# Kernel optimization log

Measured on AMD Instinct MI355X. Metric: run time of the kernel, lower is better.

Reference implementation:

```python
import jax, jax.numpy as jnp
import numpy as np

N_DIRS = 32  # number of projection directions


def gram_schmidt(x):
    # x: [B, n, D]; sequential Gram-Schmidt; normalized basis vectors are
    # detached (stop_gradient) as in the torch original.
    B, n, D = x.shape
    xs = jnp.swapaxes(x, 0, 1)  # [n, B, D]
    basis0 = jnp.zeros((n, B, D), dtype=x.dtype)

    def step(carry, w):
        basis, i = carry

        def proj(j, wv):
            b = basis[j]  # rows >= i are zero and contribute nothing
            return wv - b * jnp.sum(wv * b, axis=-1, keepdims=True)

        w_o = jax.lax.fori_loop(0, n, proj, w)
        w_sg = jax.lax.stop_gradient(w_o)
        w_hat = w_sg / jnp.linalg.norm(w_sg, axis=-1, keepdims=True)
        basis = jax.lax.dynamic_update_slice(basis, w_hat[None], (i, 0, 0))
        return (basis, i + 1), w_o

    (_, _), x_orth = jax.lax.scan(step, (basis0, jnp.int32(0)), xs)
    return jnp.swapaxes(x_orth, 0, 1)  # [B, n, D]


def setup_inputs() -> dict:
    key = jax.random.key(0)
    k = jax.random.split(key, 6)
    B = 2048
    IN_LP = 32 * 26       # 832 = linear_projection_x_dim * 26
    IMG = 28 * 28         # 784
    IN_NET = 2 * IMG      # 1568
    OUT_NET = N_DIRS * IMG  # 25088

    x_distorted = jax.random.normal(k[0], (B, IN_LP), dtype=jnp.float32)
    x_restored = jax.random.uniform(k[1], (B, 1, 28, 28), dtype=jnp.float32)

    s1 = 1.0 / np.sqrt(IN_LP)
    W_lp = jax.random.uniform(k[2], (IMG, IN_LP), jnp.float32, -s1, s1)
    b_lp = jax.random.uniform(k[3], (IMG,), jnp.float32, -s1, s1)

    s2 = 1.0 / np.sqrt(IN_NET)
    W_net = jax.random.uniform(k[4], (OUT_NET, IN_NET), jnp.float32, -s2, s2)
    b_net = jax.random.uniform(k[5], (OUT_NET,), jnp.float32, -s2, s2)

    return {"x_distorted": x_distorted, "x_restored": x_restored,
            "W_lp": W_lp, "b_lp": b_lp, "W_net": W_net, "b_net": b_net}


def reference(x_distorted, x_restored, W_lp, b_lp, W_net, b_net):
    B = x_distorted.shape[0]
    xd = x_distorted.reshape(B, -1) @ W_lp.T + b_lp      # [B, 784]
    xd = xd.reshape(B, 1, 28, 28)
    x = jnp.concatenate([xd, x_restored], axis=1)        # [B, 2, 28, 28]
    x = (x - 0.5) / 0.2
    w_mat = (x.reshape(B, -1) @ W_net.T + b_net) * 0.2   # [B, n_dirs*784]
    w_mat = w_mat.reshape(B, N_DIRS, -1)                 # [B, n_dirs, 784]
    return gram_schmidt(w_mat)
```

## Files before the change

kernel.cpp:

```cpp
#include <hip/hip_runtime.h>
#include <hip/hip_bf16.h>
#include <stdint.h>


typedef short s16x8 __attribute__((ext_vector_type(8)));
typedef float f32x4 __attribute__((ext_vector_type(4)));

#define GL_LDS16(gptr, lptr)                                                   \
    __builtin_amdgcn_global_load_lds(                                          \
        (const __attribute__((address_space(1))) void*)(gptr),                 \
        (__attribute__((address_space(3))) void*)(lptr), 16, 0, 0)

#define KP 1600

__global__ __launch_bounds__(512, 1) void gemm_mfma_256(
    const __hip_bfloat16* __restrict__ A, const __hip_bfloat16* __restrict__ B,
    const float* __restrict__ bias, float* __restrict__ C,
    int M, int N, int K)
{
    __shared__ __align__(16) short lds[2][32768];

    const int t = threadIdx.x;
    const int l = t & 63;
    const int wv = t >> 6;
    const int wm = wv >> 2;
    const int wn = wv & 3;

    const int f  = blockIdx.x;
    const int xb = f >> 3;
    const int yb = f & 7;
    const int m0 = yb * 256;
    const int n0 = xb * 256;

    const short* As = (const short*)A;
    const short* Bs = (const short*)B;

    const int colE = (((l & 7) ^ (l >> 3)) << 3);
    const size_t aSrc0 = (size_t)(m0 +   0 + wv * 8 + (l >> 3)) * KP + colE;
    const size_t aSrc1 = (size_t)(m0 + 128 + wv * 8 + (l >> 3)) * KP + colE;
    const size_t bSrc0 = (size_t)(n0 +   0 + wv * 8 + (l >> 3)) * KP + colE;
    const size_t bSrc1 = (size_t)(n0 + 128 + wv * 8 + (l >> 3)) * KP + colE;
    const int dstW = wv * 512;

    const int sk0 = (((l >> 4) << 3)) ^ ((l & 7) << 3);
    const int sk1 = sk0 ^ 32;
    const int aBase = wm * 8192 + (l & 15) * 64;
    const int bBase = 16384 + (wn >> 1) * 8192 +
                      ((wn & 1) * 64 + (l & 15)) * 64;

    f32x4 acc[8][4] = {};

#define STAGE_TILE(buf, T)                                                     \
    do {                                                                       \
        short* d_ = &lds[buf][0];                                              \
        const size_t ko_ = (size_t)(T) * 64;                                   \
        GL_LDS16(As + aSrc0 + ko_,            d_ + dstW);                      \
        GL_LDS16(As + aSrc0 + 64 * KP + ko_,  d_ + dstW + 4096);               \
        GL_LDS16(As + aSrc1 + ko_,            d_ + dstW + 8192);               \
        GL_LDS16(As + aSrc1 + 64 * KP + ko_,  d_ + dstW + 12288);              \
        GL_LDS16(Bs + bSrc0 + ko_,            d_ + dstW + 16384);              \
        GL_LDS16(Bs + bSrc0 + 64 * KP + ko_,  d_ + dstW + 20480);              \
        GL_LDS16(Bs + bSrc1 + ko_,            d_ + dstW + 24576);              \
        GL_LDS16(Bs + bSrc1 + 64 * KP + ko_,  d_ + dstW + 28672);              \
    } while (0)

    const int NT = K >> 6;
    STAGE_TILE(0, 0);
    __syncthreads();

    for (int kt = 0; kt < NT; ++kt) {
        const int cur = kt & 1;
        const short* bufc = &lds[cur][0];

        if (kt + 1 < NT) STAGE_TILE(cur ^ 1, kt + 1);

        s16x8 bfr[4][2];
        #pragma unroll
        for (int ni = 0; ni < 4; ++ni) {
            bfr[ni][0] = *(const s16x8*)&bufc[bBase + ni * 1024 + sk0];
            bfr[ni][1] = *(const s16x8*)&bufc[bBase + ni * 1024 + sk1];
        }

        #pragma unroll
        for (int half = 0; half < 2; ++half) {
            s16x8 afr[4][2];
            #pragma unroll
            for (int mi = 0; mi < 4; ++mi) {
                const int ro = (half * 64 + mi * 16) * 64;
                afr[mi][0] = *(const s16x8*)&bufc[aBase + ro + sk0];
                afr[mi][1] = *(const s16x8*)&bufc[aBase + ro + sk1];
            }
            __builtin_amdgcn_s_setprio(1);
            #pragma unroll
            for (int mi = 0; mi < 4; ++mi)
                #pragma unroll
                for (int ni = 0; ni < 4; ++ni) {
                    acc[half * 4 + mi][ni] =
                        __builtin_amdgcn_mfma_f32_16x16x32_bf16(
                            afr[mi][0], bfr[ni][0], acc[half * 4 + mi][ni],
                            0, 0, 0);
                    acc[half * 4 + mi][ni] =
                        __builtin_amdgcn_mfma_f32_16x16x32_bf16(
                            afr[mi][1], bfr[ni][1], acc[half * 4 + mi][ni],
                            0, 0, 0);
                }
            __builtin_amdgcn_s_setprio(0);
        }

        __syncthreads();
    }
#undef STAGE_TILE

    const int row0 = m0 + wm * 128 + ((l >> 4) << 2);
    const int col0 = n0 + wn * 64 + (l & 15);
    #pragma unroll
    for (int ni = 0; ni < 4; ++ni) {
        const int n = col0 + ni * 16;
        const float bn = bias[n];
        #pragma unroll
        for (int mi = 0; mi < 8; ++mi) {
            const int r0 = row0 + mi * 16;
            #pragma unroll
            for (int r = 0; r < 4; ++r)
                C[(size_t)(r0 + r) * N + n] = (acc[mi][ni][r] + bn) * 0.2f;
        }
    }
}

__global__ __launch_bounds__(256) void wnet_to_bf16(
    const float* __restrict__ in, __hip_bfloat16* __restrict__ out)
{
    const size_t r = blockIdx.x;
    const int t = threadIdx.x;
    const float* src = in + r * 1568;
    __hip_bfloat16* dst = out + r * KP;

    for (int i = t; i < 392; i += 256) {
        float4 v = *(const float4*)(src + (i << 2));
        __hip_bfloat16 o[4] = {
            __float2bfloat16(v.x), __float2bfloat16(v.y),
            __float2bfloat16(v.z), __float2bfloat16(v.w)};
        *(ushort4*)&dst[i << 2] = *(const ushort4*)o;
    }
    if (t < 8)
        *(ushort4*)&dst[1568 + (t << 2)] = make_ushort4(0, 0, 0, 0);
}

#define TILE_M 64
#define TILE_N 64
#define TILE_K 16
#define LDS_STRIDE 72

__global__ __launch_bounds__(256) void gemm_nt_lp(
    const float* __restrict__ A, const float* __restrict__ B,
    const float* __restrict__ bias, __hip_bfloat16* __restrict__ C,
    int M, int N, int K, int ldc)
{
    __shared__ float As[TILE_K][LDS_STRIDE];
    __shared__ float Bsh[TILE_K][LDS_STRIDE];

    const int t  = threadIdx.x;
    const int tx = t & 15;
    const int ty = t >> 4;
    const int m0 = blockIdx.y * TILE_M;
    const int n0 = blockIdx.x * TILE_N;
    const int lrow = t >> 2;
    const int lk   = (t & 3) << 2;

    float acc[4][4] = {};

    for (int kt = 0; kt < K; kt += TILE_K) {
        float4 av = *(const float4*)(A + (size_t)(m0 + lrow) * K + kt + lk);
        float4 bv = make_float4(0.f, 0.f, 0.f, 0.f);
        if (n0 + lrow < N)
            bv = *(const float4*)(B + (size_t)(n0 + lrow) * K + kt + lk);

        __syncthreads();
        As[lk + 0][lrow] = av.x; As[lk + 1][lrow] = av.y;
        As[lk + 2][lrow] = av.z; As[lk + 3][lrow] = av.w;
        Bsh[lk + 0][lrow] = bv.x; Bsh[lk + 1][lrow] = bv.y;
        Bsh[lk + 2][lrow] = bv.z; Bsh[lk + 3][lrow] = bv.w;
        __syncthreads();

        #pragma unroll
        for (int k = 0; k < TILE_K; ++k) {
            float4 a = *(const float4*)&As[k][ty << 2];
            float4 b = *(const float4*)&Bsh[k][tx << 2];
            acc[0][0] += a.x * b.x; acc[0][1] += a.x * b.y;
            acc[0][2] += a.x * b.z; acc[0][3] += a.x * b.w;
            acc[1][0] += a.y * b.x; acc[1][1] += a.y * b.y;
            acc[1][2] += a.y * b.z; acc[1][3] += a.y * b.w;
            acc[2][0] += a.z * b.x; acc[2][1] += a.z * b.y;
            acc[2][2] += a.z * b.z; acc[2][3] += a.z * b.w;
            acc[3][0] += a.w * b.x; acc[3][1] += a.w * b.y;
            acc[3][2] += a.w * b.z; acc[3][3] += a.w * b.w;
        }
    }

    #pragma unroll
    for (int j = 0; j < 4; ++j) {
        int n = n0 + (tx << 2) + j;
        if (n < N) {
            float bn = bias[n];
            #pragma unroll
            for (int i = 0; i < 4; ++i) {
                float v = (acc[i][j] + bn - 0.5f) / 0.2f;
                C[(size_t)(m0 + (ty << 2) + i) * ldc + n] = __float2bfloat16(v);
            }
        }
    }
}

__global__ __launch_bounds__(256) void build_restored(
    const float* __restrict__ xr, __hip_bfloat16* __restrict__ x)
{
    const int b = blockIdx.x;
    const int t = threadIdx.x;
    if (t < 196) {
        float4 v = *(const float4*)(xr + (size_t)b * 784 + (t << 2));
        __hip_bfloat16 o[4] = {
            __float2bfloat16((v.x - 0.5f) / 0.2f),
            __float2bfloat16((v.y - 0.5f) / 0.2f),
            __float2bfloat16((v.z - 0.5f) / 0.2f),
            __float2bfloat16((v.w - 0.5f) / 0.2f)};
        *(ushort4*)&x[(size_t)b * KP + 784 + (t << 2)] = *(const ushort4*)o;
    } else if (t < 204) {
        *(ushort4*)&x[(size_t)b * KP + 1568 + ((t - 196) << 2)] =
            make_ushort4(0, 0, 0, 0);
    }
}

#define GS_N 32
#define GS_D 784

__global__ __launch_bounds__(256, 4) void gram_solve(
    const float* __restrict__ out, float* __restrict__ Mws)
{
    __shared__ __align__(16) short Wc[GS_N * 64];
    __shared__ float Gs[GS_N][GS_N + 1];
    __shared__ float Ms[GS_N][GS_N + 1];
    __shared__ float Ld[GS_N];

    const int t = threadIdx.x;
    const int l = t & 63;
    const int w = t >> 6;
    const float* row0 = out + (size_t)blockIdx.x * (GS_N * GS_D);

    const int wr = w >> 1, wc2 = w & 1;
    const int ra = wr * 16 + (l & 15);
    const int rb = wc2 * 16 + (l & 15);
    const int kg = l >> 4;

    f32x4 acc = {};

    for (int k0 = 0; k0 < 832; k0 += 64) {
        #pragma unroll
        for (int hh = 0; hh < 2; ++hh) {
            const int h   = t + hh * 256;
            const int r   = h >> 4;
            const int hg  = h & 15;
            const int col = k0 + (hg << 2);
            ushort4 u = make_ushort4(0, 0, 0, 0);
            if (col < GS_D) {
                float4 v = *(const float4*)(row0 + r * GS_D + col);
                __hip_bfloat16 hb[4] = {
                    __float2bfloat16(v.x), __float2bfloat16(v.y),
                    __float2bfloat16(v.z), __float2bfloat16(v.w)};
                u = *(const ushort4*)hb;
            }
            const int gp = (hg >> 1) ^ (r & 7);
            *(ushort4*)&Wc[(r << 6) + (gp << 3) + ((hg & 1) << 2)] = u;
        }
        __syncthreads();

        #pragma unroll
        for (int s = 0; s < 2; ++s) {
            const int ga = ((s << 2) + kg) ^ (ra & 7);
            const int gb = ((s << 2) + kg) ^ (rb & 7);
            s16x8 af = *(const s16x8*)&Wc[(ra << 6) + (ga << 3)];
            s16x8 bf = *(const s16x8*)&Wc[(rb << 6) + (gb << 3)];
            acc = __builtin_amdgcn_mfma_f32_16x16x32_bf16(af, bf, acc, 0, 0, 0);
        }
        __syncthreads();
    }

    {
        const int di = wr * 16 + (l >> 4) * 4;
        const int dj = wc2 * 16 + (l & 15);
        #pragma unroll
        for (int r = 0; r < 4; ++r) Gs[di + r][dj] = acc[r];
    }
    for (int z = t; z < GS_N * (GS_N + 1); z += 256) ((float*)Ms)[z] = 0.f;
    __syncthreads();

    for (int k = 0; k < GS_N; ++k) {
        const float sk = sqrtf(Gs[k][k]);
        if (t == k) Ld[k] = sk;
        if (t > k && t < GS_N) Gs[t][k] /= sk;
        __syncthreads();
        if (t > k && t < GS_N) {
            const float lik = Gs[t][k];
            for (int j = k + 1; j <= t; ++j)
                Gs[t][j] -= lik * Gs[j][k];
        }
        __syncthreads();
    }

    if (t < GS_N) {
        const int j = t;
        Ms[j][j] = 1.0f / Ld[j];
        for (int i = j + 1; i < GS_N; ++i) {
            float a = 0.f;
            for (int k = j; k < i; ++k)
                a += Gs[i][k] * Ms[k][j];
            Ms[i][j] = -a / Ld[i];
        }
        for (int i = j + 1; i < GS_N; ++i)
            Ms[i][j] *= Ld[i];
    }
    __syncthreads();

    {
        const int i = t >> 3, j0 = (t & 7) << 2;
        float4 mv = make_float4(Ms[i][j0], Ms[i][j0 + 1],
                                Ms[i][j0 + 2], Ms[i][j0 + 3]);
        *(float4*)(Mws + (size_t)blockIdx.x * 1024 + (t << 2)) = mv;
    }
}

__global__ __launch_bounds__(256, 8) void gs_apply(
    float* __restrict__ out, const float* __restrict__ Mws)
{
    __shared__ float4 Wf[GS_N][28];
    __shared__ float  Ml[GS_N][36];

    const int t = threadIdx.x;
    const int b = blockIdx.y;
    const int k0 = blockIdx.x * 112;
    float* row0 = out + (size_t)b * (GS_N * GS_D);

    {
        float4 mv = *(const float4*)(Mws + (size_t)b * 1024 + (t << 2));
        const int i = t >> 3, j0 = (t & 7) << 2;
        *(float4*)&Ml[i][j0] = mv;
    }
    #pragma unroll
    for (int hh = 0; hh < 4; ++hh) {
        const int h = t + hh * 256;
        const int r = h >> 5, c = h & 31;
        if (c < 28)
            Wf[r][c] = *(const float4*)(row0 + r * GS_D + k0 + (c << 2));
    }
    __syncthreads();

    const int rg = t >> 5;
    const int c4 = t & 31;
    if (c4 < 28) {
        const int i0 = rg << 2;
        float4 c0 = Wf[i0 + 0][c4];
        float4 c1 = Wf[i0 + 1][c4];
        float4 c2 = Wf[i0 + 2][c4];
        float4 c3 = Wf[i0 + 3][c4];
        for (int j = 0; j < GS_N - 1; ++j) {
            if (j > i0 + 2) break;
            const float4 wj = Wf[j][c4];
            const float m0 = (i0 + 0 > j) ? Ml[i0 + 0][j] : 0.f;
            const float m1 = (i0 + 1 > j) ? Ml[i0 + 1][j] : 0.f;
            const float m2 = (i0 + 2 > j) ? Ml[i0 + 2][j] : 0.f;
            const float m3 = (i0 + 3 > j) ? Ml[i0 + 3][j] : 0.f;
            c0.x += m0 * wj.x; c0.y += m0 * wj.y;
            c0.z += m0 * wj.z; c0.w += m0 * wj.w;
            c1.x += m1 * wj.x; c1.y += m1 * wj.y;
            c1.z += m1 * wj.z; c1.w += m1 * wj.w;
            c2.x += m2 * wj.x; c2.y += m2 * wj.y;
            c2.z += m2 * wj.z; c2.w += m2 * wj.w;
            c3.x += m3 * wj.x; c3.y += m3 * wj.y;
            c3.z += m3 * wj.z; c3.w += m3 * wj.w;
        }
        *(float4*)(row0 + (i0 + 0) * GS_D + k0 + (c4 << 2)) = c0;
        *(float4*)(row0 + (i0 + 1) * GS_D + k0 + (c4 << 2)) = c1;
        *(float4*)(row0 + (i0 + 2) * GS_D + k0 + (c4 << 2)) = c2;
        *(float4*)(row0 + (i0 + 3) * GS_D + k0 + (c4 << 2)) = c3;
    }
}

extern "C" void kernel_launch(void* const* d_in, const int* in_sizes, int n_in,
                              void* d_out, int out_size, void* d_ws, size_t ws_size,
                              hipStream_t stream)
{
    const float* xd   = (const float*)d_in[0];
    const float* xr   = (const float*)d_in[1];
    const float* Wlp  = (const float*)d_in[2];
    const float* blp  = (const float*)d_in[3];
    const float* Wnet = (const float*)d_in[4];
    const float* bnet = (const float*)d_in[5];
    float* out = (float*)d_out;

    const int B = 2048, IN_LP = 832, IMG = 784, OUT = 32 * 784;

    __hip_bfloat16* Wnet_bf = (__hip_bfloat16*)d_ws;
    __hip_bfloat16* x_bf =
        (__hip_bfloat16*)((char*)d_ws + (size_t)OUT * KP * 2);
    float* Mws = (float*)d_ws;

    wnet_to_bf16<<<OUT, 256, 0, stream>>>(Wnet, Wnet_bf);

    gemm_nt_lp<<<dim3((IMG + TILE_N - 1) / TILE_N, B / TILE_M), 256, 0, stream>>>(
        xd, Wlp, blp, x_bf, B, IMG, IN_LP, KP);

    build_restored<<<B, 256, 0, stream>>>(xr, x_bf);

    gemm_mfma_256<<<dim3(784), 512, 0, stream>>>(
        x_bf, Wnet_bf, bnet, out, B, OUT, KP);

    gram_solve<<<B, 256, 0, stream>>>(out, Mws);

    gs_apply<<<dim3(7, B), 256, 0, stream>>>(out, Mws);
}
```

Baseline: 455.7 us.

## Retile main GEMM to 256x224 blocks and balance triangular GS apply work

Changes the big MFMA GEMM tile from 256x256 to 256x224, so N=25088 splits into 112 column blocks and the grid becomes 896 blocks. Warps are rearranged as 4x2 with 64x112 sub-tiles, and the A and B loads are split so half the waves stage A and half stage B. The gs_apply kernel now pairs rows i with 31-i so each thread gets a balanced share of the triangular update, instead of giving the bottom row groups more work. This trades some per-block reuse and adds a tail of extra blocks for finer tiling, aiming for better CU balance (896 blocks on 256 CUs) and less divergence.

After: 448.1 us. About the same (-1.7%).

```diff
diff --git a/kernel.cpp b/kernel.cpp
--- a/kernel.cpp
+++ b/kernel.cpp
@@ -18,50 +18,50 @@
     const float* __restrict__ bias, float* __restrict__ C,
     int M, int N, int K)
 {
-    __shared__ __align__(16) short lds[2][32768];
+    __shared__ __align__(16) short lds[2][30720];
 
     const int t = threadIdx.x;
     const int l = t & 63;
     const int wv = t >> 6;
-    const int wm = wv >> 2;
-    const int wn = wv & 3;
+    const int wm = wv >> 1;
+    const int wn = wv & 1;
 
     const int f  = blockIdx.x;
     const int xb = f >> 3;
     const int yb = f & 7;
     const int m0 = yb * 256;
-    const int n0 = xb * 256;
+    const int n0 = xb * 224;
 
     const short* As = (const short*)A;
     const short* Bs = (const short*)B;
 
+    const bool isA = wv < 4;
     const int colE = (((l & 7) ^ (l >> 3)) << 3);
-    const size_t aSrc0 = (size_t)(m0 +   0 + wv * 8 + (l >> 3)) * KP + colE;
-    const size_t aSrc1 = (size_t)(m0 + 128 + wv * 8 + (l >> 3)) * KP + colE;
-    const size_t bSrc0 = (size_t)(n0 +   0 + wv * 8 + (l >> 3)) * KP + colE;
-    const size_t bSrc1 = (size_t)(n0 + 128 + wv * 8 + (l >> 3)) * KP + colE;
-    const int dstW = wv * 512;
-
-    const int sk0 = (((l >> 4) << 3)) ^ ((l & 7) << 3);
+    const size_t srcRow = isA ? (size_t)(m0 + wv * 64 + (l >> 3))
+                              : (size_t)(n0 + (wv - 4) * 56 + (l >> 3));
+    const size_t src0 = srcRow * KP + colE;
+    const short* gsrc = isA ? As : Bs;
+    const int dstBase = isA ? wv * 4096 : 16384 + (wv - 4) * 3584;
+
+    const int sk0 = ((l >> 4) << 3) ^ ((l & 7) << 3);
     const int sk1 = sk0 ^ 32;
-    const int aBase = wm * 8192 + (l & 15) * 64;
-    const int bBase = 16384 + (wn >> 1) * 8192 +
-                      ((wn & 1) * 64 + (l & 15)) * 64;
-
-    f32x4 acc[8][4] = {};
+    const int aoff = (wm * 64 + (l & 15)) * 64;
+    const int boff = 16384 + (wn * 112 + (l & 15)) * 64;
+
+    f32x4 acc[4][7] = {};
 
 #define STAGE_TILE(buf, T)                                                     \
     do {                                                                       \
-        short* d_ = &lds[buf][0];                                              \
-        const size_t ko_ = (size_t)(T) * 64;                                   \
-        GL_LDS16(As + aSrc0 + ko_,            d_ + dstW);                      \
-        GL_LDS16(As + aSrc0 + 64 * KP + ko_,  d_ + dstW + 4096);               \
-        GL_LDS16(As + aSrc1 + ko_,            d_ + dstW + 8192);               \
-        GL_LDS16(As + aSrc1 + 64 * KP + ko_,  d_ + dstW + 12288);              \
-        GL_LDS16(Bs + bSrc0 + ko_,            d_ + dstW + 16384);              \
-        GL_LDS16(Bs + bSrc0 + 64 * KP + ko_,  d_ + dstW + 20480);              \
-        GL_LDS16(Bs + bSrc1 + ko_,            d_ + dstW + 24576);              \
-        GL_LDS16(Bs + bSrc1 + 64 * KP + ko_,  d_ + dstW + 28672);              \
+        short* d_ = &lds[buf][dstBase];                                        \
+        const short* s_ = gsrc + src0 + (size_t)(T) * 64;                      \
+        GL_LDS16(s_ + (size_t)0 * 8 * KP, d_ + 0 * 512);                       \
+        GL_LDS16(s_ + (size_t)1 * 8 * KP, d_ + 1 * 512);                       \
+        GL_LDS16(s_ + (size_t)2 * 8 * KP, d_ + 2 * 512);                       \
+        GL_LDS16(s_ + (size_t)3 * 8 * KP, d_ + 3 * 512);                       \
+        GL_LDS16(s_ + (size_t)4 * 8 * KP, d_ + 4 * 512);                       \
+        GL_LDS16(s_ + (size_t)5 * 8 * KP, d_ + 5 * 512);                       \
+        GL_LDS16(s_ + (size_t)6 * 8 * KP, d_ + 6 * 512);                       \
+        if (isA) GL_LDS16(s_ + (size_t)7 * 8 * KP, d_ + 7 * 512);              \
     } while (0)
 
     const int NT = K >> 6;
@@ -74,36 +74,25 @@
 
         if (kt + 1 < NT) STAGE_TILE(cur ^ 1, kt + 1);
 
-        s16x8 bfr[4][2];
-        #pragma unroll
-        for (int ni = 0; ni < 4; ++ni) {
-            bfr[ni][0] = *(const s16x8*)&bufc[bBase + ni * 1024 + sk0];
-            bfr[ni][1] = *(const s16x8*)&bufc[bBase + ni * 1024 + sk1];
-        }
-
-        #pragma unroll
-        for (int half = 0; half < 2; ++half) {
-            s16x8 afr[4][2];
-            #pragma unroll
-            for (int mi = 0; mi < 4; ++mi) {
-                const int ro = (half * 64 + mi * 16) * 64;
-                afr[mi][0] = *(const s16x8*)&bufc[aBase + ro + sk0];
-                afr[mi][1] = *(const s16x8*)&bufc[aBase + ro + sk1];
-            }
+        s16x8 bfr[7][2];
+        #pragma unroll
+        for (int ni = 0; ni < 7; ++ni) {
+            bfr[ni][0] = *(const s16x8*)&bufc[boff + ni * 1024 + sk0];
+            bfr[ni][1] = *(const s16x8*)&bufc[boff + ni * 1024 + sk1];
+        }
+
+        #pragma unroll
+        for (int mi = 0; mi < 4; ++mi) {
+            s16x8 a0 = *(const s16x8*)&bufc[aoff + mi * 1024 + sk0];
+            s16x8 a1 = *(const s16x8*)&bufc[aoff + mi * 1024 + sk1];
             __builtin_amdgcn_s_setprio(1);
             #pragma unroll
-            for (int mi = 0; mi < 4; ++mi)
-                #pragma unroll
-                for (int ni = 0; ni < 4; ++ni) {
-                    acc[half * 4 + mi][ni] =
-                        __builtin_amdgcn_mfma_f32_16x16x32_bf16(
-                            afr[mi][0], bfr[ni][0], acc[half * 4 + mi][ni],
-                            0, 0, 0);
-                    acc[half * 4 + mi][ni] =
-                        __builtin_amdgcn_mfma_f32_16x16x32_bf16(
-                            afr[mi][1], bfr[ni][1], acc[half * 4 + mi][ni],
-                            0, 0, 0);
-                }
+            for (int ni = 0; ni < 7; ++ni) {
+                acc[mi][ni] = __builtin_amdgcn_mfma_f32_16x16x32_bf16(
+                    a0, bfr[ni][0], acc[mi][ni], 0, 0, 0);
+                acc[mi][ni] = __builtin_amdgcn_mfma_f32_16x16x32_bf16(
+                    a1, bfr[ni][1], acc[mi][ni], 0, 0, 0);
+            }
             __builtin_amdgcn_s_setprio(0);
         }
 
@@ -111,14 +100,14 @@
     }
 #undef STAGE_TILE
 
-    const int row0 = m0 + wm * 128 + ((l >> 4) << 2);
-    const int col0 = n0 + wn * 64 + (l & 15);
+    const int row0 = m0 + wm * 64 + ((l >> 4) << 2);
+    const int col0 = n0 + wn * 112 + (l & 15);
     #pragma unroll
-    for (int ni = 0; ni < 4; ++ni) {
+    for (int ni = 0; ni < 7; ++ni) {
         const int n = col0 + ni * 16;
         const float bn = bias[n];
         #pragma unroll
-        for (int mi = 0; mi < 8; ++mi) {
+        for (int mi = 0; mi < 4; ++mi) {
             const int r0 = row0 + mi * 16;
             #pragma unroll
             for (int r = 0; r < 4; ++r)
@@ -353,34 +342,36 @@
     }
     __syncthreads();
 
-    const int rg = t >> 5;
+    const int g  = t >> 5;
     const int c4 = t & 31;
     if (c4 < 28) {
-        const int i0 = rg << 2;
-        float4 c0 = Wf[i0 + 0][c4];
-        float4 c1 = Wf[i0 + 1][c4];
-        float4 c2 = Wf[i0 + 2][c4];
-        float4 c3 = Wf[i0 + 3][c4];
-        for (int j = 0; j < GS_N - 1; ++j) {
-            if (j > i0 + 2) break;
+        const int rA = g, rB = 31 - g, rC = 15 - g, rD = 16 + g;
+        float4 vA = Wf[rA][c4];
+        float4 vB = Wf[rB][c4];
+        float4 vC = Wf[rC][c4];
+        float4 vD = Wf[rD][c4];
+        for (int j = 0; j < rB; ++j) {
             const float4 wj = Wf[j][c4];
-            const float m0 = (i0 + 0 > j) ? Ml[i0 + 0][j] : 0.f;
-            const float m1 = (i0 + 1 > j) ? Ml[i0 + 1][j] : 0.f;
-            const float m2 = (i0 + 2 > j) ? Ml[i0 + 2][j] : 0.f;
-            const float m3 = (i0 + 3 > j) ? Ml[i0 + 3][j] : 0.f;
-            c0.x += m0 * wj.x; c0.y += m0 * wj.y;
-            c0.z += m0 * wj.z; c0.w += m0 * wj.w;
-            c1.x += m1 * wj.x; c1.y += m1 * wj.y;
-            c1.z += m1 * wj.z; c1.w += m1 * wj.w;
-            c2.x += m2 * wj.x; c2.y += m2 * wj.y;
-            c2.z += m2 * wj.z; c2.w += m2 * wj.w;
-            c3.x += m3 * wj.x; c3.y += m3 * wj.y;
-            c3.z += m3 * wj.z; c3.w += m3 * wj.w;
-        }
-        *(float4*)(row0 + (i0 + 0) * GS_D + k0 + (c4 << 2)) = c0;
-        *(float4*)(row0 + (i0 + 1) * GS_D + k0 + (c4 << 2)) = c1;
-        *(float4*)(row0 + (i0 + 2) * GS_D + k0 + (c4 << 2)) = c2;
-        *(float4*)(row0 + (i0 + 3) * GS_D + k0 + (c4 << 2)) = c3;
+            const float mA = (j < rA) ? Ml[rA][j] : 0.f;
+            const float mB = Ml[rB][j];
+            vA.x += mA * wj.x; vA.y += mA * wj.y;
+            vA.z += mA * wj.z; vA.w += mA * wj.w;
+            vB.x += mB * wj.x; vB.y += mB * wj.y;
+            vB.z += mB * wj.z; vB.w += mB * wj.w;
+        }
+        for (int j = 0; j < rD; ++j) {
+            const float4 wj = Wf[j][c4];
+            const float mC = (j < rC) ? Ml[rC][j] : 0.f;
+            const float mD = Ml[rD][j];
+            vC.x += mC * wj.x; vC.y += mC * wj.y;
+            vC.z += mC * wj.z; vC.w += mC * wj.w;
+            vD.x += mD * wj.x; vD.y += mD * wj.y;
+            vD.z += mD * wj.z; vD.w += mD * wj.w;
+        }
+        *(float4*)(row0 + rA * GS_D + k0 + (c4 << 2)) = vA;
+        *(float4*)(row0 + rB * GS_D + k0 + (c4 << 2)) = vB;
+        *(float4*)(row0 + rC * GS_D + k0 + (c4 << 2)) = vC;
+        *(float4*)(row0 + rD * GS_D + k0 + (c4 << 2)) = vD;
     }
 }
 
@@ -410,7 +401,7 @@
 
     build_restored<<<B, 256, 0, stream>>>(xr, x_bf);
 
-    gemm_mfma_256<<<dim3(784), 512, 0, stream>>>(
+    gemm_mfma_256<<<dim3(896), 512, 0, stream>>>(
         x_bf, Wnet_bf, bnet, out, B, OUT, KP);
 
     gram_solve<<<B, 256, 0, stream>>>(out, Mws);
```
